# Performance work log

Hardware: AMD Instinct MI355X
Metric: run time of the kernel (lower is better)

Reference implementation:

```python
import jax, jax.numpy as jnp
import numpy as np

D_MODEL = 128
K_RED = 3          # fd_redundancy_k
MAX_ITERS = 16     # upper bound on the data-dependent while-loop; masked no-ops after convergence
NEG = -1e9


def setup_inputs() -> dict:
    key = jax.random.key(0)
    ks = jax.random.split(key, 10)
    B, U, S, D, F = 16, 2048, 512, D_MODEL, 32
    return {
        "user_enc": jax.random.normal(ks[0], (B, U, D), jnp.float32),
        "server_enc": jax.random.normal(ks[1], (B, S, D), jnp.float32),
        "users": jax.random.uniform(ks[2], (B, U, 6), jnp.float32),
        "servers": jax.random.uniform(ks[3], (B, S, 7), jnp.float32),
        "connect": jax.random.randint(ks[4], (B, U, S), 0, 2, jnp.int32),
        "fd_onehot": jax.random.randint(ks[5], (B, S, F), 0, 2, jnp.int32),
        "state_proj_w": jax.random.normal(ks[6], (D, 4), jnp.float32) * 0.05,
        "state_proj_b": jnp.zeros((D,), jnp.float32),
        "fd_bias": jnp.asarray(1.0, jnp.float32),
        "ptr_q_w": jax.random.normal(ks[7], (D, D), jnp.float32) * (D ** -0.5),
        "ptr_k_w": jax.random.normal(ks[8], (D, D), jnp.float32) * (D ** -0.5),
        "user_state_w": jax.random.normal(ks[9], (1, 3), jnp.float32) * 0.05,
        "score_bias": jnp.zeros((1,), jnp.float32),
    }


def _forward(user_enc, server_enc, users, servers, connect, fd_onehot,
             state_proj_w, state_proj_b, fd_bias, ptr_q_w, ptr_k_w,
             user_state_w, score_bias):
    B, U, _ = users.shape
    S = servers.shape[1]
    D = user_enc.shape[-1]
    needs = users[..., 2:6]                    # [B,U,4]
    init_cap = servers[..., 3:7]               # [B,S,4]
    connect_mask = connect.astype(bool)
    fd = fd_onehot.astype(jnp.float32)         # [B,S,F] in {0,1}
    F = fd.shape[-1]
    inv_sqrt_d = D ** -0.5
    tk = jnp.float32(max(K_RED, 1))
    q = user_enc @ ptr_q_w.T                   # [B,U,D]  (loop-invariant)
    u_ids = jnp.arange(U)
    s_ids = jnp.arange(S)

    def body(carry, _):
        alloc, cap, seen, logp, flag = carry
        replica_count = alloc.sum(-1)                                    # [B,U]
        need_more = replica_count < K_RED
        can_fulfill = jnp.all(cap[:, None] >= needs[:, :, None], axis=-1)  # [B,U,S]
        eligible = connect_mask & can_fulfill & need_more[..., None] & ~alloc
        go = flag & jnp.any(need_more) & jnp.any(eligible)

        # pointer-attention logits with dynamic server state
        is_new_fd = (jnp.einsum('buf,bsf->bus', seen, fd) < 0.5).astype(jnp.float32)
        cap_ratio = cap / jnp.maximum(init_cap, 1e-6)
        k_vec = (server_enc + cap_ratio @ state_proj_w.T + state_proj_b) @ ptr_k_w.T
        logits = jnp.einsum('bud,bsd->bus', q, k_vec) * inv_sqrt_d + score_bias
        logits = logits + fd_bias * is_new_fd
        rc = replica_count.astype(jnp.float32)
        user_state = jnp.stack([rc / tk,
                                jnp.clip(K_RED - rc, 0.0, None) / tk,
                                (replica_count == K_RED - 1).astype(jnp.float32)], axis=-1)
        logits = logits + user_state @ user_state_w.T                    # broadcast [B,U,1]

        cand = jnp.where(eligible, logits, NEG)
        # each valid server greedily proposes its best eligible user
        valid_server = jnp.any(eligible, axis=1)                         # [B,S]
        prop_u = jnp.argmax(cand, axis=1)                                # [B,S]
        prop_mask = valid_server[:, None, :] & (u_ids[None, :, None] == prop_u[:, None, :])
        logp_prop = jnp.max(cand, axis=1) - jax.nn.logsumexp(cand, axis=1)  # [B,S]

        # each proposed user accepts the highest-scoring proposing server
        acc_cand = jnp.where(prop_mask, logits, NEG)
        has_prop = jnp.any(prop_mask, axis=2)                            # [B,U]
        chosen_s = jnp.argmax(acc_cand, axis=2)                          # [B,U]
        accepted = has_prop[..., None] & (s_ids == chosen_s[..., None])  # [B,U,S]

        alloc = alloc | (accepted & go)
        fd_gain = (jnp.einsum('bus,bsf->buf', prop_mask.astype(jnp.float32), fd) > 0).astype(jnp.float32)
        seen = jnp.where(go, jnp.maximum(seen, fd_gain), seen)
        used = jnp.einsum('bus,buc->bsc', accepted.astype(jnp.float32), needs)
        cap = jnp.where(go, jnp.maximum(cap - used, 0.0), cap)
        gathered = jnp.take_along_axis(logp_prop, chosen_s, axis=1)      # [B,U]
        logp = logp + jnp.where(go & has_prop, gathered, 0.0)
        return (alloc, cap, seen, logp, go), None

    init = (jnp.zeros((B, U, S), bool), init_cap,
            jnp.zeros((B, U, F), jnp.float32), jnp.zeros((B, U), jnp.float32),
            jnp.asarray(True))
    (alloc, cap, seen, logp, _), _ = jax.lax.scan(body, init, None, length=MAX_ITERS)
    return logp.sum(axis=1), alloc, cap


def reference(user_enc, server_enc, users, servers, connect, fd_onehot,
              state_proj_w, state_proj_b, fd_bias, ptr_q_w, ptr_k_w,
              user_state_w, score_bias):
    # policy='greedy' branch of the original forward
    return _forward(user_enc, server_enc, users, servers, connect, fd_onehot,
                    state_proj_w, state_proj_b, fd_bias, ptr_q_w, ptr_k_w,
                    user_state_w, score_bias)
```

## Files before the change

kernel.cpp:

```cpp
#include <hip/hip_runtime.h>
#include <hip/hip_bf16.h>

#define B_N 16
#define U_N 2048
#define S_N 512
#define D_N 128
#define INV_SQRT_D 0.08838834764831845f

typedef unsigned long long ull;
typedef __attribute__((ext_vector_type(8))) short bf16x8;
typedef __attribute__((ext_vector_type(4))) float f32x4;
typedef __attribute__((ext_vector_type(4))) _Float16 f16x4;

__device__ __forceinline__ unsigned monof(float v) {
    unsigned b = __float_as_uint(v);
    return (b & 0x80000000u) ? ~b : (b | 0x80000000u);
}
__device__ __forceinline__ float unmonof(unsigned m) {
    unsigned b = (m & 0x80000000u) ? (m & 0x7fffffffu) : ~m;
    return __uint_as_float(b);
}
__device__ __forceinline__ unsigned short f2bf(float x) {
    unsigned u = __float_as_uint(x);
    return (unsigned short)((u + 0x7fffu + ((u >> 16) & 1u)) >> 16);
}

__global__ void init_state(const float* __restrict__ servers, const float* __restrict__ users,
                           const int* __restrict__ fd_onehot,
                           unsigned* allocU, uint4* alloc3, unsigned* rcArr, unsigned* seenArr,
                           float* logp, float* capA, float* invA, unsigned* fdm, float* nds,
                           unsigned* any_valid) {
    int i = blockIdx.x * 256 + threadIdx.x;
    if (i < B_N * U_N * 16) allocU[i] = 0u;
    if (i < B_N * U_N) {
        rcArr[i] = 0u; seenArr[i] = 0u; logp[i] = 0.f;
        alloc3[i] = make_uint4(0xFFFFFFFFu, 0xFFFFFFFFu, 0xFFFFFFFFu, 0xFFFFFFFFu);
        const float* up = users + (size_t)i * 6;
        nds[i * 4 + 0] = up[2]; nds[i * 4 + 1] = up[3];
        nds[i * 4 + 2] = up[4]; nds[i * 4 + 3] = up[5];
    }
    if (i < B_N * S_N) {
        const float* sp = servers + (size_t)i * 7;
        float4 c = make_float4(sp[3], sp[4], sp[5], sp[6]);
        ((float4*)capA)[i] = c;
        ((float4*)invA)[i] = make_float4(1.f / fmaxf(c.x, 1e-6f), 1.f / fmaxf(c.y, 1e-6f),
                                         1.f / fmaxf(c.z, 1e-6f), 1.f / fmaxf(c.w, 1e-6f));
        unsigned w = 0u;
        const int* fp = fd_onehot + (size_t)i * 32;
        #pragma unroll
        for (int f = 0; f < 32; ++f) w |= (fp[f] != 0 ? 1u : 0u) << f;
        fdm[i] = w;
    }
    if (i < 16) any_valid[i] = 0u;
}

__global__ void pack_connect(const int* __restrict__ connect, ull* __restrict__ connU) {
    int i = blockIdx.x * 4 + (threadIdx.x >> 6);
    int lane = threadIdx.x & 63;
    const int* row = connect + (size_t)i * S_N;
    #pragma unroll
    for (int c = 0; c < 8; ++c) {
        ull m = __ballot(row[c * 64 + lane] != 0);
        if (lane == 0) connU[(size_t)i * 8 + c] = m;
    }
}

template <bool ABIAS, int OUTMODE>
__global__ __launch_bounds__(256) void gemm_nt(const float* __restrict__ A, const float* __restrict__ Bm,
                                               const float* __restrict__ abias, float* __restrict__ C,
                                               unsigned short* __restrict__ C16,
                                               int M, int N, int K, float scale) {
    __shared__ float As[16][68];
    __shared__ float Bs[16][68];
    int z = blockIdx.z;
    const float* Ab = A + (size_t)z * M * K;
    const float* Bb = Bm;
    int m0 = blockIdx.x * 64, n0 = blockIdx.y * 64;
    int tid = threadIdx.x;
    int tx = tid & 15, ty = tid >> 4;
    int lrow = tid >> 2, lk = (tid & 3) * 4;
    float acc[4][4] = {};
    for (int k0 = 0; k0 < K; k0 += 16) {
        float4 av = *(const float4*)(Ab + (size_t)(m0 + lrow) * K + k0 + lk);
        float4 bv = *(const float4*)(Bb + (size_t)(n0 + lrow) * K + k0 + lk);
        if (ABIAS) {
            av.x += abias[k0 + lk]; av.y += abias[k0 + lk + 1];
            av.z += abias[k0 + lk + 2]; av.w += abias[k0 + lk + 3];
        }
        __syncthreads();
        As[lk + 0][lrow] = av.x; As[lk + 1][lrow] = av.y; As[lk + 2][lrow] = av.z; As[lk + 3][lrow] = av.w;
        Bs[lk + 0][lrow] = bv.x; Bs[lk + 1][lrow] = bv.y; Bs[lk + 2][lrow] = bv.z; Bs[lk + 3][lrow] = bv.w;
        __syncthreads();
        #pragma unroll
        for (int kk = 0; kk < 16; ++kk) {
            float4 a = *(const float4*)&As[kk][ty * 4];
            float4 bq = *(const float4*)&Bs[kk][tx * 4];
            float ar[4] = {a.x, a.y, a.z, a.w}, br[4] = {bq.x, bq.y, bq.z, bq.w};
            #pragma unroll
            for (int ii = 0; ii < 4; ++ii)
                #pragma unroll
                for (int jj = 0; jj < 4; ++jj) acc[ii][jj] += ar[ii] * br[jj];
        }
    }
    #pragma unroll
    for (int ii = 0; ii < 4; ++ii) {
        float4 o = make_float4(acc[ii][0] * scale, acc[ii][1] * scale,
                               acc[ii][2] * scale, acc[ii][3] * scale);
        size_t idx = (size_t)z * M * N + (size_t)(m0 + ty * 4 + ii) * N + n0 + tx * 4;
        if (OUTMODE != 1) *(float4*)(C + idx) = o;
        if (OUTMODE != 0) {
            ushort4 ob;
            ob.x = f2bf(o.x); ob.y = f2bf(o.y); ob.z = f2bf(o.z); ob.w = f2bf(o.w);
            *(ushort4*)(C16 + idx) = ob;
        }
    }
}

__global__ void m2_kernel(const float* __restrict__ kw, const float* __restrict__ spw, float* __restrict__ M2) {
    int t = threadIdx.x;
    if (t < 512) {
        int d = t >> 2, c = t & 3;
        float acc = 0.f;
        for (int e = 0; e < 128; ++e) acc += kw[d * 128 + e] * spw[e * 4 + c];
        M2[t] = acc * INV_SQRT_D;
    }
}

__global__ void qm_kernel(const float* __restrict__ q, const float* __restrict__ M2, float* __restrict__ qm) {
    __shared__ float qs[64][129];
    __shared__ float m2s[512];
    int b = blockIdx.y, u0 = blockIdx.x * 64;
    int t = threadIdx.x;
    for (int i = t; i < 512; i += 256) m2s[i] = M2[i];
    #pragma unroll
    for (int it = 0; it < 8; ++it) {
        int f4 = t + 256 * it;
        int row = f4 >> 5;
        int col = (f4 & 31) * 4;
        float4 v = *(const float4*)(q + ((size_t)(b * U_N + u0 + row)) * D_N + col);
        qs[row][col] = v.x; qs[row][col + 1] = v.y; qs[row][col + 2] = v.z; qs[row][col + 3] = v.w;
    }
    __syncthreads();
    int ul = t >> 2, c = t & 3;
    float acc = 0.f;
    for (int d = 0; d < 128; ++d) acc += qs[ul][d] * m2s[d * 4 + c];
    qm[((size_t)(b * U_N + u0 + ul)) * 4 + c] = acc;
}

__global__ __launch_bounds__(256) void qk_mfma(const unsigned short* __restrict__ qb,
                                               const unsigned short* __restrict__ kb,
                                               _Float16* __restrict__ qkh) {
    const int b = blockIdx.z, u0 = blockIdx.x * 128, s0 = blockIdx.y * 64;
    const int t = threadIdx.x, w = t >> 6, l = t & 63;
    const int lr = l & 15, lq = l >> 4;
    const unsigned short* Ab = qb + ((size_t)(b * U_N + u0 + w * 32 + lr)) * D_N + lq * 8;
    const unsigned short* Bb = kb + ((size_t)(b * S_N + s0 + lr)) * D_N + lq * 8;
    f32x4 acc[2][4] = {};
    #pragma unroll
    for (int kt = 0; kt < 4; ++kt) {
        bf16x8 a0 = *(const bf16x8*)(Ab + kt * 32);
        bf16x8 a1 = *(const bf16x8*)(Ab + 16 * D_N + kt * 32);
        #pragma unroll
        for (int c = 0; c < 4; ++c) {
            bf16x8 bf = *(const bf16x8*)(Bb + c * 16 * D_N + kt * 32);
            acc[0][c] = __builtin_amdgcn_mfma_f32_16x16x32_bf16(a0, bf, acc[0][c], 0, 0, 0);
            acc[1][c] = __builtin_amdgcn_mfma_f32_16x16x32_bf16(a1, bf, acc[1][c], 0, 0, 0);
        }
    }
    __shared__ _Float16 Cs[128][72];
    #pragma unroll
    for (int mt = 0; mt < 2; ++mt)
        #pragma unroll
        for (int c = 0; c < 4; ++c)
            #pragma unroll
            for (int r = 0; r < 4; ++r)
                Cs[w * 32 + mt * 16 + lq * 4 + r][c * 16 + lr] = (_Float16)acc[mt][c][r];
    __syncthreads();
    #pragma unroll
    for (int k = 0; k < 4; ++k) {
        int row = (t >> 3) + k * 32;
        int sg = (t & 7) * 8;
        uint4 v = *(const uint4*)&Cs[row][sg];
        *(uint4*)(qkh + ((size_t)(b * U_N + u0 + row)) * S_N + s0 + sg) = v;
    }
}

__global__ __launch_bounds__(256) void iter_score(
    const _Float16* __restrict__ qkh, const float* __restrict__ qm4,
    const float* __restrict__ nds, const unsigned* __restrict__ connU32,
    const uint4* __restrict__ alloc3, const unsigned* __restrict__ rcArr,
    const unsigned* __restrict__ seenArr, const unsigned* __restrict__ fdm_,
    const float* __restrict__ capA, const float* __restrict__ invA,
    const float* __restrict__ usw, const float* __restrict__ sbp, const float* __restrict__ fdbp,
    ull* __restrict__ keypart, float* __restrict__ sumpart,
    const unsigned* __restrict__ any_valid, int iter) {
    if (iter > 0 && any_valid[iter - 1] == 0u) return;
    const int tid = threadIdx.x;
    const int b = blockIdx.x & 15;
    const int ublk = blockIdx.x >> 4;
    const int u0 = ublk << 5;
    const int h = tid >> 7;
    const int sl = tid & 127;
    const int s0 = sl * 4;
    const float w0 = usw[0], w1 = usw[1], w2 = usw[2], sb = sbp[0], fdb = fdbp[0];
    const float ub0 = sb + w1;
    const float ub1 = sb + w0 * (1.f / 3.f) + w1 * (2.f / 3.f);
    const float ub2 = sb + w0 * (2.f / 3.f) + w1 * (1.f / 3.f) + w2;
    const int bsb = b * S_N + s0;
    float4 cap[4], cr[4]; unsigned fq[4];
    #pragma unroll
    for (int j = 0; j < 4; ++j) {
        cap[j] = ((const float4*)capA)[bsb + j];
        float4 iv = ((const float4*)invA)[bsb + j];
        cr[j] = make_float4(cap[j].x * iv.x, cap[j].y * iv.y, cap[j].z * iv.z, cap[j].w * iv.w);
        fq[j] = fdm_[bsb + j];
    }
    ull k[4] = {0ULL, 0ULL, 0ULL, 0ULL};
    float e[4] = {0.f, 0.f, 0.f, 0.f};
    const int gub = b * U_N + u0 + h * 16;
    const _Float16* qkbase = qkh + ((size_t)gub) * S_N + s0;
    const int cwbase = gub * 16 + (sl >> 3);
    const int nsh = (sl & 7) * 4;
    #pragma unroll 2
    for (int uu = 0; uu < 16; ++uu) {
        const int gu = gub + uu;
        const unsigned rcu = rcArr[gu];
        if (rcu < 3u) {
            const f16x4 qv = *(const f16x4*)(qkbase + (size_t)uu * S_N);
            const float4 qmv = ((const float4*)qm4)[gu];
            const float4 ndv = ((const float4*)nds)[gu];
            const unsigned snu = seenArr[gu];
            const uint4 al = alloc3[gu];
            const unsigned nib = connU32[cwbase + uu * 16] >> nsh;
            const float add = (rcu == 0u) ? ub0 : ((rcu == 1u) ? ub1 : ub2);
            const unsigned uinv = ~(unsigned)(u0 + h * 16 + uu);
            #pragma unroll
            for (int j = 0; j < 4; ++j) {
                const unsigned us = (unsigned)(s0 + j);
                const bool ful = (cap[j].x >= ndv.x) & (cap[j].y >= ndv.y) &
                                 (cap[j].z >= ndv.z) & (cap[j].w >= ndv.w);
                const bool aok = (al.x != us) & (al.y != us) & (al.z != us);
                const bool el = (((nib >> j) & 1u) != 0u) & ful & aok;
                const float lg = (float)qv[j] + qmv.x * cr[j].x + qmv.y * cr[j].y +
                                 qmv.z * cr[j].z + qmv.w * cr[j].w + add +
                                 (((snu & fq[j]) == 0u) ? fdb : 0.f);
                if (el) {
                    const ull kk = ((ull)monof(lg) << 32) | uinv;
                    k[j] = k[j] > kk ? k[j] : kk;
                    e[j] += __expf(lg);
                }
            }
        }
    }
    __shared__ ull mk[128][4];
    __shared__ float me[128][4];
    if (h == 1) {
        #pragma unroll
        for (int j = 0; j < 4; ++j) { mk[sl][j] = k[j]; me[sl][j] = e[j]; }
    }
    __syncthreads();
    if (h == 0) {
        #pragma unroll
        for (int j = 0; j < 4; ++j) {
            const ull o = mk[sl][j];
            k[j] = o > k[j] ? o : k[j];
            e[j] += me[sl][j];
        }
        const size_t p = (size_t)ublk * (B_N * S_N) + bsb;
        ulonglong2 ka; ka.x = k[0]; ka.y = k[1];
        ulonglong2 kc; kc.x = k[2]; kc.y = k[3];
        *(ulonglong2*)(keypart + p) = ka;
        *(ulonglong2*)(keypart + p + 2) = kc;
        *(float4*)(sumpart + p) = make_float4(e[0], e[1], e[2], e[3]);
    }
}

__global__ __launch_bounds__(1024) void iter_midapply(
    const ull* __restrict__ keypart, const float* __restrict__ sumpart,
    const unsigned* __restrict__ fdm_, const float* __restrict__ nds,
    uint4* __restrict__ alloc3, unsigned* __restrict__ allocU,
    unsigned* __restrict__ rcArr, unsigned* __restrict__ seenArr,
    float* __restrict__ capA, float* __restrict__ logp,
    unsigned* __restrict__ any_valid, int iter) {
    if (iter > 0 && any_valid[iter - 1] == 0u) return;
    __shared__ ull ukeyL[2048];
    __shared__ unsigned sgL[2048];
    __shared__ ull bkL[512];
    __shared__ float bsL[512];
    __shared__ float lpL[512];
    const int b = blockIdx.x, t = threadIdx.x;
    ukeyL[t] = 0ULL; ukeyL[t + 1024] = 0ULL;
    sgL[t] = 0u; sgL[t + 1024] = 0u;
    __syncthreads();
    const int s = t & 511, h = t >> 9;
    const int base = b * S_N + s;
    ull best = 0ULL; float ssum = 0.f;
    #pragma unroll 16
    for (int j = h * 32; j < h * 32 + 32; ++j) {
        const ull kk = keypart[(size_t)j * (B_N * S_N) + base];
        best = kk > best ? kk : best;
        ssum += sumpart[(size_t)j * (B_N * S_N) + base];
    }
    if (h == 0) { bkL[s] = best; bsL[s] = ssum; }
    __syncthreads();
    unsigned prop = 0u;
    if (h == 1) {
        const ull ob = bkL[s];
        best = ob > best ? ob : best;
        ssum += bsL[s];
        if (best != 0ULL) {
            const float mx = unmonof((unsigned)(best >> 32));
            const unsigned pu = ~(unsigned)best;
            lpL[s] = mx - __logf(ssum);
            const ull pk = ((ull)monof(mx) << 32) | (~(unsigned)s);
            atomicMax(&ukeyL[pu], pk);
            atomicOr(&sgL[pu], fdm_[base]);
            prop = 1u;
        }
    }
    const ull bal = __ballot(prop != 0u);
    if (bal != 0ULL && (t & 63) == 0) atomicOr(&any_valid[iter], 1u);
    __syncthreads();
    #pragma unroll
    for (int g = 0; g < 2; ++g) {
        const int u = t + g * 1024;
        const ull key = ukeyL[u];
        if (key != 0ULL) {
            const int gu = b * U_N + u;
            const unsigned s2 = ~(unsigned)key;
            const int bs2 = b * S_N + (int)s2;
            uint4 al = alloc3[gu];
            const unsigned r = rcArr[gu];
            if (r == 0u) al.x = s2; else if (r == 1u) al.y = s2; else al.z = s2;
            alloc3[gu] = al;
            allocU[gu * 16 + (s2 >> 5)] |= 1u << (s2 & 31u);
            const float4 nd = ((const float4*)nds)[gu];
            float4 cv = ((float4*)capA)[bs2];
            cv.x = fmaxf(cv.x - nd.x, 0.f); cv.y = fmaxf(cv.y - nd.y, 0.f);
            cv.z = fmaxf(cv.z - nd.z, 0.f); cv.w = fmaxf(cv.w - nd.w, 0.f);
            ((float4*)capA)[bs2] = cv;
            rcArr[gu] = r + 1u;
            logp[gu] += lpL[s2];
            seenArr[gu] |= sgL[u];
        }
    }
}

__global__ void finalize_logp(const float* __restrict__ logp, float* __restrict__ out) {
    int b = blockIdx.x, t = threadIdx.x;
    float s = 0.f;
    for (int u = t; u < U_N; u += 256) s += logp[b * U_N + u];
    #pragma unroll
    for (int m = 1; m < 64; m <<= 1) s += __shfl_xor(s, m, 64);
    __shared__ float r[4];
    if ((t & 63) == 0) r[t >> 6] = s;
    __syncthreads();
    if (t == 0) out[b] = r[0] + r[1] + r[2] + r[3];
}

__global__ void finalize_alloc(const unsigned* __restrict__ allocU, float* __restrict__ out) {
    int idx = blockIdx.x * 256 + threadIdx.x;
    int bu = idx >> 7;
    int s4 = (idx & 127) * 4;
    unsigned w = allocU[bu * 16 + (s4 >> 5)];
    float4 o;
    o.x = ((w >> ((s4 + 0) & 31)) & 1u) ? 1.f : 0.f;
    o.y = ((w >> ((s4 + 1) & 31)) & 1u) ? 1.f : 0.f;
    o.z = ((w >> ((s4 + 2) & 31)) & 1u) ? 1.f : 0.f;
    o.w = ((w >> ((s4 + 3) & 31)) & 1u) ? 1.f : 0.f;
    *(float4*)(out + 16 + (size_t)bu * S_N + s4) = o;
}

__global__ void finalize_cap(const float* __restrict__ capA, float* __restrict__ out) {
    int i = blockIdx.x * 256 + threadIdx.x;
    if (i < B_N * S_N * 4) out[16 + (size_t)B_N * U_N * S_N + i] = capA[i];
}

extern "C" void kernel_launch(void* const* d_in, const int* in_sizes, int n_in,
                              void* d_out, int out_size, void* d_ws, size_t ws_size,
                              hipStream_t stream) {
    const float* user_enc = (const float*)d_in[0];
    const float* server_enc = (const float*)d_in[1];
    const float* users = (const float*)d_in[2];
    const float* servers = (const float*)d_in[3];
    const int* connect = (const int*)d_in[4];
    const int* fd_onehot = (const int*)d_in[5];
    const float* state_proj_w = (const float*)d_in[6];
    const float* state_proj_b = (const float*)d_in[7];
    const float* fd_bias = (const float*)d_in[8];
    const float* ptr_q_w = (const float*)d_in[9];
    const float* ptr_k_w = (const float*)d_in[10];
    const float* user_state_w = (const float*)d_in[11];
    const float* score_bias = (const float*)d_in[12];
    float* out = (float*)d_out;

    char* w = (char*)d_ws;
    _Float16* qkh = (_Float16*)(w + 0);
    float* q = (float*)(w + 33554432);
    unsigned short* qb = (unsigned short*)(w + 50331648);
    unsigned short* kb = (unsigned short*)(w + 58720256);
    ull* keypart = (ull*)(w + 60817408);
    float* sumpart = (float*)(w + 65011712);
    float* qm = (float*)(w + 67108864);
    ull* connU = (ull*)(w + 67633152);
    unsigned* allocU = (unsigned*)(w + 69730304);
    uint4* alloc3 = (uint4*)(w + 71827456);
    float* nds = (float*)(w + 72351744);
    unsigned* fdm = (unsigned*)(w + 72876032);
    float* capA = (float*)(w + 72908800);
    float* invA = (float*)(w + 73039872);
    unsigned* rcArr = (unsigned*)(w + 73170944);
    unsigned* seenArr = (unsigned*)(w + 73302016);
    float* logp = (float*)(w + 73433088);
    float* M2 = (float*)(w + 73564160);
    unsigned* any_valid = (unsigned*)(w + 73566208);

    init_state<<<2048, 256, 0, stream>>>(servers, users, fd_onehot, allocU, alloc3, rcArr,
                                         seenArr, logp, capA, invA, fdm, nds, any_valid);
    pack_connect<<<8192, 256, 0, stream>>>(connect, connU);
    gemm_nt<true, 1><<<dim3(8, 2, 16), 256, 0, stream>>>(server_enc, ptr_k_w, state_proj_b,
                                                         nullptr, kb, S_N, D_N, D_N, INV_SQRT_D);
    gemm_nt<false, 2><<<dim3(32, 2, 16), 256, 0, stream>>>(user_enc, ptr_q_w, nullptr,
                                                           q, qb, U_N, D_N, D_N, 1.0f);
    m2_kernel<<<1, 512, 0, stream>>>(ptr_k_w, state_proj_w, M2);
    qm_kernel<<<dim3(32, 16), 256, 0, stream>>>(q, M2, qm);
    qk_mfma<<<dim3(16, 8, 16), 256, 0, stream>>>(qb, kb, qkh);
    for (int it = 0; it < 16; ++it) {
        iter_score<<<1024, 256, 0, stream>>>(qkh, qm, nds, (const unsigned*)connU, alloc3, rcArr,
                                             seenArr, fdm, capA, invA, user_state_w, score_bias,
                                             fd_bias, keypart, sumpart, any_valid, it);
        iter_midapply<<<16, 1024, 0, stream>>>(keypart, sumpart, fdm, nds, alloc3, allocU,
                                               rcArr, seenArr, capA, logp, any_valid, it);
    }
    finalize_logp<<<16, 256, 0, stream>>>(logp, out);
    finalize_alloc<<<16384, 256, 0, stream>>>(allocU, out);
    finalize_cap<<<128, 256, 0, stream>>>(capA, out);
}
```

Measured before the change: 498.2 us.

## Fuse per-iteration score and apply kernels via last-block reduction, merge setup kernels

```diff
diff --git a/kernel.cpp b/kernel.cpp
--- a/kernel.cpp
+++ b/kernel.cpp
@@ -25,11 +25,22 @@
     return (unsigned short)((u + 0x7fffu + ((u >> 16) & 1u)) >> 16);
 }
 
-__global__ void init_state(const float* __restrict__ servers, const float* __restrict__ users,
-                           const int* __restrict__ fd_onehot,
-                           unsigned* allocU, uint4* alloc3, unsigned* rcArr, unsigned* seenArr,
-                           float* logp, float* capA, float* invA, unsigned* fdm, float* nds,
-                           unsigned* any_valid) {
+__global__ void init_pack(const float* __restrict__ servers, const float* __restrict__ users,
+                          const int* __restrict__ fd_onehot, const int* __restrict__ connect,
+                          ull* __restrict__ connU,
+                          unsigned* allocU, uint4* alloc3, unsigned* rcArr, unsigned* seenArr,
+                          float* logp, float* capA, float* invA, unsigned* fdm, float* nds,
+                          unsigned* any_valid, unsigned* done_cnt) {
+    {
+        int r = blockIdx.x * 4 + (threadIdx.x >> 6);
+        int lane = threadIdx.x & 63;
+        const int* row = connect + (size_t)r * S_N;
+        #pragma unroll
+        for (int c = 0; c < 8; ++c) {
+            ull m = __ballot(row[c * 64 + lane] != 0);
+            if (lane == 0) connU[(size_t)r * 8 + c] = m;
+        }
+    }
     int i = blockIdx.x * 256 + threadIdx.x;
     if (i < B_N * U_N * 16) allocU[i] = 0u;
     if (i < B_N * U_N) {
@@ -51,41 +62,38 @@
         for (int f = 0; f < 32; ++f) w |= (fp[f] != 0 ? 1u : 0u) << f;
         fdm[i] = w;
     }
+    if (i < 256) done_cnt[i] = 0u;
     if (i < 16) any_valid[i] = 0u;
 }
 
-__global__ void pack_connect(const int* __restrict__ connect, ull* __restrict__ connU) {
-    int i = blockIdx.x * 4 + (threadIdx.x >> 6);
-    int lane = threadIdx.x & 63;
-    const int* row = connect + (size_t)i * S_N;
-    #pragma unroll
-    for (int c = 0; c < 8; ++c) {
-        ull m = __ballot(row[c * 64 + lane] != 0);
-        if (lane == 0) connU[(size_t)i * 8 + c] = m;
-    }
-}
-
-template <bool ABIAS, int OUTMODE>
-__global__ __launch_bounds__(256) void gemm_nt(const float* __restrict__ A, const float* __restrict__ Bm,
-                                               const float* __restrict__ abias, float* __restrict__ C,
-                                               unsigned short* __restrict__ C16,
-                                               int M, int N, int K, float scale) {
+__global__ __launch_bounds__(256) void gemm_both(const float* __restrict__ user_enc,
+                                                 const float* __restrict__ server_enc,
+                                                 const float* __restrict__ spb,
+                                                 const float* __restrict__ qw,
+                                                 const float* __restrict__ kw,
+                                                 float* __restrict__ q,
+                                                 unsigned short* __restrict__ qb,
+                                                 unsigned short* __restrict__ kb) {
     __shared__ float As[16][68];
     __shared__ float Bs[16][68];
-    int z = blockIdx.z;
-    const float* Ab = A + (size_t)z * M * K;
-    const float* Bb = Bm;
-    int m0 = blockIdx.x * 64, n0 = blockIdx.y * 64;
-    int tid = threadIdx.x;
-    int tx = tid & 15, ty = tid >> 4;
-    int lrow = tid >> 2, lk = (tid & 3) * 4;
+    const int z = blockIdx.z;
+    const bool isK = blockIdx.x < 8;
+    const int xb = isK ? blockIdx.x : blockIdx.x - 8;
+    const int M = isK ? S_N : U_N;
+    const float* Ab = (isK ? server_enc : user_enc) + (size_t)z * M * D_N;
+    const float* Bb = isK ? kw : qw;
+    const float scale = isK ? INV_SQRT_D : 1.0f;
+    const int m0 = xb * 64, n0 = blockIdx.y * 64;
+    const int tid = threadIdx.x;
+    const int tx = tid & 15, ty = tid >> 4;
+    const int lrow = tid >> 2, lk = (tid & 3) * 4;
     float acc[4][4] = {};
-    for (int k0 = 0; k0 < K; k0 += 16) {
-        float4 av = *(const float4*)(Ab + (size_t)(m0 + lrow) * K + k0 + lk);
-        float4 bv = *(const float4*)(Bb + (size_t)(n0 + lrow) * K + k0 + lk);
-        if (ABIAS) {
-            av.x += abias[k0 + lk]; av.y += abias[k0 + lk + 1];
-            av.z += abias[k0 + lk + 2]; av.w += abias[k0 + lk + 3];
+    for (int k0 = 0; k0 < D_N; k0 += 16) {
+        float4 av = *(const float4*)(Ab + (size_t)(m0 + lrow) * D_N + k0 + lk);
+        float4 bv = *(const float4*)(Bb + (size_t)(n0 + lrow) * D_N + k0 + lk);
+        if (isK) {
+            const float4 sv = *(const float4*)(spb + k0 + lk);
+            av.x += sv.x; av.y += sv.y; av.z += sv.z; av.w += sv.w;
         }
         __syncthreads();
         As[lk + 0][lrow] = av.x; As[lk + 1][lrow] = av.y; As[lk + 2][lrow] = av.z; As[lk + 3][lrow] = av.w;
@@ -106,32 +114,26 @@
     for (int ii = 0; ii < 4; ++ii) {
         float4 o = make_float4(acc[ii][0] * scale, acc[ii][1] * scale,
                                acc[ii][2] * scale, acc[ii][3] * scale);
-        size_t idx = (size_t)z * M * N + (size_t)(m0 + ty * 4 + ii) * N + n0 + tx * 4;
-        if (OUTMODE != 1) *(float4*)(C + idx) = o;
-        if (OUTMODE != 0) {
-            ushort4 ob;
-            ob.x = f2bf(o.x); ob.y = f2bf(o.y); ob.z = f2bf(o.z); ob.w = f2bf(o.w);
-            *(ushort4*)(C16 + idx) = ob;
-        }
-    }
-}
-
-__global__ void m2_kernel(const float* __restrict__ kw, const float* __restrict__ spw, float* __restrict__ M2) {
-    int t = threadIdx.x;
-    if (t < 512) {
-        int d = t >> 2, c = t & 3;
-        float acc = 0.f;
-        for (int e = 0; e < 128; ++e) acc += kw[d * 128 + e] * spw[e * 4 + c];
-        M2[t] = acc * INV_SQRT_D;
-    }
-}
-
-__global__ void qm_kernel(const float* __restrict__ q, const float* __restrict__ M2, float* __restrict__ qm) {
+        size_t idx = (size_t)z * M * D_N + (size_t)(m0 + ty * 4 + ii) * D_N + n0 + tx * 4;
+        ushort4 ob;
+        ob.x = f2bf(o.x); ob.y = f2bf(o.y); ob.z = f2bf(o.z); ob.w = f2bf(o.w);
+        if (isK) {
+            *(ushort4*)(kb + idx) = ob;
+        } else {
+            *(float4*)(q + idx) = o;
+            *(ushort4*)(qb + idx) = ob;
+        }
+    }
+}
+
+__global__ void qm_kernel(const float* __restrict__ q, const float* __restrict__ kw,
+                          const float* __restrict__ spw, float* __restrict__ qm) {
     __shared__ float qs[64][129];
     __shared__ float m2s[512];
+    __shared__ float sps[512];
     int b = blockIdx.y, u0 = blockIdx.x * 64;
     int t = threadIdx.x;
-    for (int i = t; i < 512; i += 256) m2s[i] = M2[i];
+    for (int i = t; i < 512; i += 256) sps[i] = spw[i];
     #pragma unroll
     for (int it = 0; it < 8; ++it) {
         int f4 = t + 256 * it;
@@ -139,6 +141,13 @@
         int col = (f4 & 31) * 4;
         float4 v = *(const float4*)(q + ((size_t)(b * U_N + u0 + row)) * D_N + col);
         qs[row][col] = v.x; qs[row][col + 1] = v.y; qs[row][col + 2] = v.z; qs[row][col + 3] = v.w;
+    }
+    __syncthreads();
+    for (int i = t; i < 512; i += 256) {
+        int d = i >> 2, c = i & 3;
+        float a = 0.f;
+        for (int e = 0; e < 128; ++e) a += kw[d * 128 + e] * sps[e * 4 + c];
+        m2s[i] = a * INV_SQRT_D;
     }
     __syncthreads();
     int ul = t >> 2, c = t & 3;
@@ -185,20 +194,21 @@
     }
 }
 
-__global__ __launch_bounds__(256) void iter_score(
+__global__ __launch_bounds__(256) void iter_fused(
     const _Float16* __restrict__ qkh, const float* __restrict__ qm4,
     const float* __restrict__ nds, const unsigned* __restrict__ connU32,
-    const uint4* __restrict__ alloc3, const unsigned* __restrict__ rcArr,
-    const unsigned* __restrict__ seenArr, const unsigned* __restrict__ fdm_,
-    const float* __restrict__ capA, const float* __restrict__ invA,
+    uint4* __restrict__ alloc3, unsigned* __restrict__ rcArr,
+    unsigned* __restrict__ seenArr, const unsigned* __restrict__ fdm_,
+    float* __restrict__ capA, const float* __restrict__ invA,
     const float* __restrict__ usw, const float* __restrict__ sbp, const float* __restrict__ fdbp,
     ull* __restrict__ keypart, float* __restrict__ sumpart,
-    const unsigned* __restrict__ any_valid, int iter) {
+    unsigned* __restrict__ allocU, float* __restrict__ logp,
+    unsigned* __restrict__ any_valid, unsigned* __restrict__ done_cnt, int iter) {
     if (iter > 0 && any_valid[iter - 1] == 0u) return;
     const int tid = threadIdx.x;
     const int b = blockIdx.x & 15;
     const int ublk = blockIdx.x >> 4;
-    const int u0 = ublk << 5;
+    const int u0 = ublk << 6;
     const int h = tid >> 7;
     const int sl = tid & 127;
     const int s0 = sl * 4;
@@ -217,12 +227,12 @@
     }
     ull k[4] = {0ULL, 0ULL, 0ULL, 0ULL};
     float e[4] = {0.f, 0.f, 0.f, 0.f};
-    const int gub = b * U_N + u0 + h * 16;
+    const int gub = b * U_N + u0 + h * 32;
     const _Float16* qkbase = qkh + ((size_t)gub) * S_N + s0;
     const int cwbase = gub * 16 + (sl >> 3);
     const int nsh = (sl & 7) * 4;
     #pragma unroll 2
-    for (int uu = 0; uu < 16; ++uu) {
+    for (int uu = 0; uu < 32; ++uu) {
         const int gu = gub + uu;
         const unsigned rcu = rcArr[gu];
         if (rcu < 3u) {
@@ -233,7 +243,7 @@
             const uint4 al = alloc3[gu];
             const unsigned nib = connU32[cwbase + uu * 16] >> nsh;
             const float add = (rcu == 0u) ? ub0 : ((rcu == 1u) ? ub1 : ub2);
-            const unsigned uinv = ~(unsigned)(u0 + h * 16 + uu);
+            const unsigned uinv = ~(unsigned)(u0 + h * 32 + uu);
             #pragma unroll
             for (int j = 0; j < 4; ++j) {
                 const unsigned us = (unsigned)(s0 + j);
@@ -273,57 +283,50 @@
         *(ulonglong2*)(keypart + p + 2) = kc;
         *(float4*)(sumpart + p) = make_float4(e[0], e[1], e[2], e[3]);
     }
-}
-
-__global__ __launch_bounds__(1024) void iter_midapply(
-    const ull* __restrict__ keypart, const float* __restrict__ sumpart,
-    const unsigned* __restrict__ fdm_, const float* __restrict__ nds,
-    uint4* __restrict__ alloc3, unsigned* __restrict__ allocU,
-    unsigned* __restrict__ rcArr, unsigned* __restrict__ seenArr,
-    float* __restrict__ capA, float* __restrict__ logp,
-    unsigned* __restrict__ any_valid, int iter) {
-    if (iter > 0 && any_valid[iter - 1] == 0u) return;
+    __syncthreads();
+    __shared__ int lastF;
+    if (tid == 0) {
+        __threadfence();
+        lastF = (atomicAdd(&done_cnt[iter * 16 + b], 1u) == 31u) ? 1 : 0;
+    }
+    __syncthreads();
+    if (!lastF) return;
+    __threadfence();
     __shared__ ull ukeyL[2048];
     __shared__ unsigned sgL[2048];
-    __shared__ ull bkL[512];
-    __shared__ float bsL[512];
     __shared__ float lpL[512];
-    const int b = blockIdx.x, t = threadIdx.x;
-    ukeyL[t] = 0ULL; ukeyL[t + 1024] = 0ULL;
-    sgL[t] = 0u; sgL[t + 1024] = 0u;
-    __syncthreads();
-    const int s = t & 511, h = t >> 9;
-    const int base = b * S_N + s;
-    ull best = 0ULL; float ssum = 0.f;
-    #pragma unroll 16
-    for (int j = h * 32; j < h * 32 + 32; ++j) {
-        const ull kk = keypart[(size_t)j * (B_N * S_N) + base];
-        best = kk > best ? kk : best;
-        ssum += sumpart[(size_t)j * (B_N * S_N) + base];
-    }
-    if (h == 0) { bkL[s] = best; bsL[s] = ssum; }
-    __syncthreads();
-    unsigned prop = 0u;
-    if (h == 1) {
-        const ull ob = bkL[s];
-        best = ob > best ? ob : best;
-        ssum += bsL[s];
+    __shared__ unsigned propF;
+    #pragma unroll
+    for (int g = 0; g < 8; ++g) { ukeyL[tid + g * 256] = 0ULL; sgL[tid + g * 256] = 0u; }
+    if (tid == 0) propF = 0u;
+    __syncthreads();
+    unsigned hasp = 0u;
+    #pragma unroll
+    for (int half = 0; half < 2; ++half) {
+        const int s = tid + half * 256;
+        const int base = b * S_N + s;
+        ull best = 0ULL; float ssum = 0.f;
+        #pragma unroll 8
+        for (int j = 0; j < 32; ++j) {
+            const ull kk = keypart[(size_t)j * (B_N * S_N) + base];
+            best = kk > best ? kk : best;
+            ssum += sumpart[(size_t)j * (B_N * S_N) + base];
+        }
         if (best != 0ULL) {
             const float mx = unmonof((unsigned)(best >> 32));
             const unsigned pu = ~(unsigned)best;
             lpL[s] = mx - __logf(ssum);
-            const ull pk = ((ull)monof(mx) << 32) | (~(unsigned)s);
-            atomicMax(&ukeyL[pu], pk);
+            atomicMax(&ukeyL[pu], ((ull)monof(mx) << 32) | (~(unsigned)s));
             atomicOr(&sgL[pu], fdm_[base]);
-            prop = 1u;
-        }
-    }
-    const ull bal = __ballot(prop != 0u);
-    if (bal != 0ULL && (t & 63) == 0) atomicOr(&any_valid[iter], 1u);
-    __syncthreads();
-    #pragma unroll
-    for (int g = 0; g < 2; ++g) {
-        const int u = t + g * 1024;
+            hasp = 1u;
+        }
+    }
+    if (hasp) atomicOr(&propF, 1u);
+    __syncthreads();
+    if (tid == 0 && propF != 0u) atomicOr(&any_valid[iter], 1u);
+    #pragma unroll
+    for (int g = 0; g < 8; ++g) {
+        const int u = tid + g * 256;
         const ull key = ukeyL[u];
         if (key != 0ULL) {
             const int gu = b * U_N + u;
@@ -346,34 +349,33 @@
     }
 }
 
-__global__ void finalize_logp(const float* __restrict__ logp, float* __restrict__ out) {
-    int b = blockIdx.x, t = threadIdx.x;
-    float s = 0.f;
-    for (int u = t; u < U_N; u += 256) s += logp[b * U_N + u];
-    #pragma unroll
-    for (int m = 1; m < 64; m <<= 1) s += __shfl_xor(s, m, 64);
-    __shared__ float r[4];
-    if ((t & 63) == 0) r[t >> 6] = s;
-    __syncthreads();
-    if (t == 0) out[b] = r[0] + r[1] + r[2] + r[3];
-}
-
-__global__ void finalize_alloc(const unsigned* __restrict__ allocU, float* __restrict__ out) {
-    int idx = blockIdx.x * 256 + threadIdx.x;
-    int bu = idx >> 7;
-    int s4 = (idx & 127) * 4;
-    unsigned w = allocU[bu * 16 + (s4 >> 5)];
-    float4 o;
-    o.x = ((w >> ((s4 + 0) & 31)) & 1u) ? 1.f : 0.f;
-    o.y = ((w >> ((s4 + 1) & 31)) & 1u) ? 1.f : 0.f;
-    o.z = ((w >> ((s4 + 2) & 31)) & 1u) ? 1.f : 0.f;
-    o.w = ((w >> ((s4 + 3) & 31)) & 1u) ? 1.f : 0.f;
-    *(float4*)(out + 16 + (size_t)bu * S_N + s4) = o;
-}
-
-__global__ void finalize_cap(const float* __restrict__ capA, float* __restrict__ out) {
-    int i = blockIdx.x * 256 + threadIdx.x;
-    if (i < B_N * S_N * 4) out[16 + (size_t)B_N * U_N * S_N + i] = capA[i];
+__global__ void finalize_all(const unsigned* __restrict__ allocU, const float* __restrict__ capA,
+                             const float* __restrict__ logp, float* __restrict__ out) {
+    const int bid = blockIdx.x, t = threadIdx.x;
+    const int idx = bid * 256 + t;
+    {
+        const int bu = idx >> 7;
+        const int s4 = (idx & 127) * 4;
+        const unsigned w = allocU[bu * 16 + (s4 >> 5)];
+        float4 o;
+        o.x = ((w >> ((s4 + 0) & 31)) & 1u) ? 1.f : 0.f;
+        o.y = ((w >> ((s4 + 1) & 31)) & 1u) ? 1.f : 0.f;
+        o.z = ((w >> ((s4 + 2) & 31)) & 1u) ? 1.f : 0.f;
+        o.w = ((w >> ((s4 + 3) & 31)) & 1u) ? 1.f : 0.f;
+        *(float4*)(out + 16 + (size_t)bu * S_N + s4) = o;
+    }
+    if (idx < B_N * S_N * 4) out[16 + (size_t)B_N * U_N * S_N + idx] = capA[idx];
+    if (bid >= 16368) {
+        const int b = bid - 16368;
+        float s = 0.f;
+        for (int u = t; u < U_N; u += 256) s += logp[b * U_N + u];
+        #pragma unroll
+        for (int m = 1; m < 64; m <<= 1) s += __shfl_xor(s, m, 64);
+        __shared__ float r[4];
+        if ((t & 63) == 0) r[t >> 6] = s;
+        __syncthreads();
+        if (t == 0) out[b] = r[0] + r[1] + r[2] + r[3];
+    }
 }
 
 extern "C" void kernel_launch(void* const* d_in, const int* in_sizes, int n_in,
@@ -400,39 +402,33 @@
     unsigned short* qb = (unsigned short*)(w + 50331648);
     unsigned short* kb = (unsigned short*)(w + 58720256);
     ull* keypart = (ull*)(w + 60817408);
-    float* sumpart = (float*)(w + 65011712);
-    float* qm = (float*)(w + 67108864);
-    ull* connU = (ull*)(w + 67633152);
-    unsigned* allocU = (unsigned*)(w + 69730304);
-    uint4* alloc3 = (uint4*)(w + 71827456);
-    float* nds = (float*)(w + 72351744);
-    unsigned* fdm = (unsigned*)(w + 72876032);
-    float* capA = (float*)(w + 72908800);
-    float* invA = (float*)(w + 73039872);
-    unsigned* rcArr = (unsigned*)(w + 73170944);
-    unsigned* seenArr = (unsigned*)(w + 73302016);
-    float* logp = (float*)(w + 73433088);
-    float* M2 = (float*)(w + 73564160);
-    unsigned* any_valid = (unsigned*)(w + 73566208);
-
-    init_state<<<2048, 256, 0, stream>>>(servers, users, fd_onehot, allocU, alloc3, rcArr,
-                                         seenArr, logp, capA, invA, fdm, nds, any_valid);
-    pack_connect<<<8192, 256, 0, stream>>>(connect, connU);
-    gemm_nt<true, 1><<<dim3(8, 2, 16), 256, 0, stream>>>(server_enc, ptr_k_w, state_proj_b,
-                                                         nullptr, kb, S_N, D_N, D_N, INV_SQRT_D);
-    gemm_nt<false, 2><<<dim3(32, 2, 16), 256, 0, stream>>>(user_enc, ptr_q_w, nullptr,
-                                                           q, qb, U_N, D_N, D_N, 1.0f);
-    m2_kernel<<<1, 512, 0, stream>>>(ptr_k_w, state_proj_w, M2);
-    qm_kernel<<<dim3(32, 16), 256, 0, stream>>>(q, M2, qm);
+    float* sumpart = (float*)(w + 62914560);
+    float* qm = (float*)(w + 63963136);
+    ull* connU = (ull*)(w + 64487424);
+    unsigned* allocU = (unsigned*)(w + 66584576);
+    uint4* alloc3 = (uint4*)(w + 68681728);
+    float* nds = (float*)(w + 69206016);
+    unsigned* fdm = (unsigned*)(w + 69730304);
+    float* capA = (float*)(w + 69763072);
+    float* invA = (float*)(w + 69894144);
+    unsigned* rcArr = (unsigned*)(w + 70025216);
+    unsigned* seenArr = (unsigned*)(w + 70156288);
+    float* logp = (float*)(w + 70287360);
+    unsigned* any_valid = (unsigned*)(w + 70418432);
+    unsigned* done_cnt = (unsigned*)(w + 70418432 + 128);
+
+    init_pack<<<8192, 256, 0, stream>>>(servers, users, fd_onehot, connect, connU,
+                                        allocU, alloc3, rcArr, seenArr, logp, capA, invA,
+                                        fdm, nds, any_valid, done_cnt);
+    gemm_both<<<dim3(40, 2, 16), 256, 0, stream>>>(user_enc, server_enc, state_proj_b,
+                                                   ptr_q_w, ptr_k_w, q, qb, kb);
+    qm_kernel<<<dim3(32, 16), 256, 0, stream>>>(q, ptr_k_w, state_proj_w, qm);
     qk_mfma<<<dim3(16, 8, 16), 256, 0, stream>>>(qb, kb, qkh);
     for (int it = 0; it < 16; ++it) {
-        iter_score<<<1024, 256, 0, stream>>>(qkh, qm, nds, (const unsigned*)connU, alloc3, rcArr,
-                                             seenArr, fdm, capA, invA, user_state_w, score_bias,
-                                             fd_bias, keypart, sumpart, any_valid, it);
-        iter_midapply<<<16, 1024, 0, stream>>>(keypart, sumpart, fdm, nds, alloc3, allocU,
-                                               rcArr, seenArr, capA, logp, any_valid, it);
-    }
-    finalize_logp<<<16, 256, 0, stream>>>(logp, out);
-    finalize_alloc<<<16384, 256, 0, stream>>>(allocU, out);
-    finalize_cap<<<128, 256, 0, stream>>>(capA, out);
-}
+        iter_fused<<<512, 256, 0, stream>>>(qkh, qm, nds, (const unsigned*)connU, alloc3, rcArr,
+                                            seenArr, fdm, capA, invA, user_state_w, score_bias,
+                                            fd_bias, keypart, sumpart, allocU, logp,
+                                            any_valid, done_cnt, it);
+    }
+    finalize_all<<<16384, 256, 0, stream>>>(allocU, capA, logp, out);
+}
```

Measured after the change: 629.4 us. +26.3%, slower.
